# Kernel optimization log

Hardware: AMD Instinct MI355X
Metric: run time of the kernel (lower is better)

Reference implementation:

```python
import jax, jax.numpy as jnp
import numpy as np

N = 100000
E = 1600000

def _gcn_layer(x, row, col, W, b):
    # gather neighbor feats then scatter-add into destination rows
    agg = jax.ops.segment_sum(x[col], row, num_segments=N)  # [N, d]
    deg = jax.ops.segment_sum(jnp.ones((row.shape[0],), x.dtype), row, num_segments=N)
    deg = jnp.clip(deg, 1.0, None)[:, None]  # [N, 1]
    return (agg / deg + x) @ W + b

def setup_inputs() -> dict:
    key = jax.random.key(0)
    ks = jax.random.split(key, 6)
    x = jax.random.normal(ks[0], (N, 64), dtype=jnp.float32)
    edge_index = jax.random.randint(ks[1], (2, E), 0, N, dtype=jnp.int64)
    W1 = jax.random.normal(ks[2], (64, 128), dtype=jnp.float32) * 0.1
    b1 = jax.random.normal(ks[3], (128,), dtype=jnp.float32) * 0.1
    W2 = jax.random.normal(ks[4], (128, 64), dtype=jnp.float32) * 0.1
    b2 = jax.random.normal(ks[5], (64,), dtype=jnp.float32) * 0.1
    return {"x": x, "edge_index": edge_index, "W1": W1, "b1": b1, "W2": W2, "b2": b2}

def reference(x, edge_index, W1, b1, W2, b2):
    row, col = edge_index[0], edge_index[1]
    h = jax.nn.relu(_gcn_layer(x, row, col, W1, b1))
    h = _gcn_layer(h, row, col, W2, b2)
    return h
```

## Files before the change

kernel.cpp:

```cpp
#include <hip/hip_runtime.h>
#include <stdint.h>

#define WS_ALIGN(x) (((x) + 255) & ~(size_t)255)
#define CSR_CAP 64
#define RPB 512
#define CAPB 9216

typedef __attribute__((ext_vector_type(8))) unsigned short ushort8_t;
typedef __attribute__((ext_vector_type(8))) short short8_t;
typedef __attribute__((ext_vector_type(4))) float float4_t;

static __device__ __forceinline__ unsigned short f2bf(float f) {
    unsigned u = __float_as_uint(f);
    unsigned r = (u + 0x7FFFu + ((u >> 16) & 1u)) >> 16;
    return (unsigned short)r;
}
static __device__ __forceinline__ float bf2f(unsigned short s) {
    return __uint_as_float(((unsigned)s) << 16);
}

__global__ void detect_idx_kernel(const int* __restrict__ p, int* __restrict__ flagOr) {
    int t = threadIdx.x;
    int v = 0;
    for (int i = t; i < 2048; i += 256) v |= p[2 * i + 1];
    if (v) atomicOr(flagOr, v);
}

__global__ void init_cursor_kernel(int* __restrict__ gCursor, int nb) {
    int i = blockIdx.x * 256 + threadIdx.x;
    if (i < nb) gCursor[i] = i * CAPB;
}

__global__ __launch_bounds__(256) void bucket_kernel(
    const void* __restrict__ eidx, int E, const int* __restrict__ flagOr,
    int nb, int* __restrict__ gCursor, int2* __restrict__ staging) {
    __shared__ int cnt[256];
    __shared__ int base[256];
    int t = threadIdx.x;
    if (t < nb) cnt[t] = 0;
    __syncthreads();

    int e0 = (blockIdx.x * 256 + t) * 8;
    bool is64 = (*flagOr == 0);
    int m = E - e0; if (m > 8) m = 8; if (m < 0) m = 0;
    int r[8], bk[8], slot[8];
    for (int j = 0; j < m; ++j) {
        r[j] = is64 ? (int)((const long long*)eidx)[e0 + j]
                    : ((const int*)eidx)[e0 + j];
        bk[j] = r[j] >> 9;
        slot[j] = atomicAdd(&cnt[bk[j]], 1);
    }
    __syncthreads();
    if (t < nb) base[t] = atomicAdd(&gCursor[t], cnt[t]);
    __syncthreads();
    for (int j = 0; j < m; ++j) {
        int c = is64 ? (int)((const long long*)eidx)[E + e0 + j]
                     : ((const int*)eidx)[E + e0 + j];
        int dst = base[bk[j]] + slot[j];
        if (dst < (bk[j] + 1) * CAPB) staging[dst] = make_int2(r[j], c);
    }
}

__global__ __launch_bounds__(1024) void ell_kernel(
    const int2* __restrict__ staging, const int* __restrict__ gCursor,
    int* __restrict__ csr, int* __restrict__ deg, int N) {
    __shared__ int lcnt[RPB];
    int b = blockIdx.x, t = threadIdx.x;
    if (t < RPB) lcnt[t] = 0;
    __syncthreads();
    int start = b * CAPB;
    int end = gCursor[b];
    if (end > start + CAPB) end = start + CAPB;
    for (int i = start + t; i < end; i += 1024) {
        int2 rc = staging[i];
        int lr = rc.x - (b << 9);
        int slot = atomicAdd(&lcnt[lr], 1);
        if (slot < CSR_CAP) csr[(size_t)rc.x * CSR_CAP + slot] = rc.y;
    }
    __syncthreads();
    int r = (b << 9) + t;
    if (t < RPB && r < N) deg[r] = lcnt[t];
}

__global__ void xcast_kernel(const float4* __restrict__ x, ushort4* __restrict__ xb,
                             int n4) {
    int i = blockIdx.x * 256 + threadIdx.x;
    if (i >= n4) return;
    float4 f = x[i];
    ushort4 o;
    o.x = f2bf(f.x); o.y = f2bf(f.y); o.z = f2bf(f.z); o.w = f2bf(f.w);
    xb[i] = o;
}

__global__ __launch_bounds__(256) void agg_kernel(
    const unsigned short* __restrict__ xb, const int* __restrict__ deg,
    const int* __restrict__ csr, unsigned short* __restrict__ v, int N) {
    int tid = threadIdx.x;
    int w = tid >> 6, lane = tid & 63;
    int oct = lane >> 3, fo = lane & 7;
    int n = blockIdx.x * 4 + w;
    if (n >= N) return;
    int d = deg[n];
    if (d > CSR_CAP) d = CSR_CAP;
    const int* row = &csr[(size_t)n * CSR_CAP];

    float a0 = 0, a1 = 0, a2 = 0, a3 = 0, a4 = 0, a5 = 0, a6 = 0, a7 = 0;
    int nIter = (d + 7) >> 3;
    int it = 0;
    for (; it + 2 <= nIter; it += 2) {
        int k0 = it * 8 + oct, k1 = k0 + 8;
        int i0 = (k0 < d) ? row[k0] : N;
        int i1 = (k1 < d) ? row[k1] : N;
        ushort8_t f0 = *(const ushort8_t*)&xb[(size_t)i0 * 64 + fo * 8];
        ushort8_t f1 = *(const ushort8_t*)&xb[(size_t)i1 * 64 + fo * 8];
        a0 += bf2f(f0[0]) + bf2f(f1[0]); a1 += bf2f(f0[1]) + bf2f(f1[1]);
        a2 += bf2f(f0[2]) + bf2f(f1[2]); a3 += bf2f(f0[3]) + bf2f(f1[3]);
        a4 += bf2f(f0[4]) + bf2f(f1[4]); a5 += bf2f(f0[5]) + bf2f(f1[5]);
        a6 += bf2f(f0[6]) + bf2f(f1[6]); a7 += bf2f(f0[7]) + bf2f(f1[7]);
    }
    if (it < nIter) {
        int k0 = it * 8 + oct;
        int i0 = (k0 < d) ? row[k0] : N;
        ushort8_t f0 = *(const ushort8_t*)&xb[(size_t)i0 * 64 + fo * 8];
        a0 += bf2f(f0[0]); a1 += bf2f(f0[1]); a2 += bf2f(f0[2]); a3 += bf2f(f0[3]);
        a4 += bf2f(f0[4]); a5 += bf2f(f0[5]); a6 += bf2f(f0[6]); a7 += bf2f(f0[7]);
    }
    #define RED(m) a0 += __shfl_xor(a0, m); a1 += __shfl_xor(a1, m); \
                   a2 += __shfl_xor(a2, m); a3 += __shfl_xor(a3, m); \
                   a4 += __shfl_xor(a4, m); a5 += __shfl_xor(a5, m); \
                   a6 += __shfl_xor(a6, m); a7 += __shfl_xor(a7, m);
    RED(8) RED(16) RED(32)
    #undef RED

    if (oct == 0) {
        ushort8_t s = *(const ushort8_t*)&xb[(size_t)n * 64 + fo * 8];
        float inv = 1.0f / (float)(d > 1 ? d : 1);
        ushort8_t o;
        o[0] = f2bf(a0 * inv + bf2f(s[0])); o[1] = f2bf(a1 * inv + bf2f(s[1]));
        o[2] = f2bf(a2 * inv + bf2f(s[2])); o[3] = f2bf(a3 * inv + bf2f(s[3]));
        o[4] = f2bf(a4 * inv + bf2f(s[4])); o[5] = f2bf(a5 * inv + bf2f(s[5]));
        o[6] = f2bf(a6 * inv + bf2f(s[6])); o[7] = f2bf(a7 * inv + bf2f(s[7]));
        *(ushort8_t*)&v[(size_t)n * 64 + fo * 8] = o;
    }
}

__global__ __launch_bounds__(256) void mlp_kernel(
    const unsigned short* __restrict__ v, const float* __restrict__ W1,
    const float* __restrict__ b1, const float* __restrict__ W2,
    unsigned short* __restrict__ g16, int N) {
    __shared__ unsigned short vA[64 * 72];
    __shared__ unsigned short W1t[128 * 72];
    __shared__ unsigned short hA[64 * 136];
    __shared__ unsigned short W2t[64 * 136];
    int t = threadIdx.x;
    int node0 = blockIdx.x * 64;

    for (int i = t; i < 1024; i += 256) {
        int node = i >> 4, k0 = (i & 15) * 4;
        int gn = node0 + node;
        ushort4 val = make_ushort4(0, 0, 0, 0);
        if (gn < N) val = *(const ushort4*)&v[(size_t)gn * 64 + k0];
        *(ushort4*)&vA[node * 72 + k0] = val;
    }
    for (int i = t; i < 8192; i += 256) {
        int k = i >> 7, col = i & 127;
        W1t[col * 72 + k] = f2bf(W1[i]);
    }
    for (int i = t; i < 8192; i += 256) {
        int k = i >> 6, col = i & 63;
        W2t[col * 136 + k] = f2bf(W2[i]);
    }
    __syncthreads();

    int w = t >> 6, lane = t & 63;
    int l15 = lane & 15, quad = lane >> 4;
    const float4_t fzero = {0.f, 0.f, 0.f, 0.f};

    short8_t af[4][2];
    #pragma unroll
    for (int ms = 0; ms < 4; ++ms)
        #pragma unroll
        for (int kk = 0; kk < 2; ++kk)
            af[ms][kk] = *(const short8_t*)&vA[(ms * 16 + l15) * 72 + kk * 32 + quad * 8];
    short8_t bf1[2][2];
    #pragma unroll
    for (int cs = 0; cs < 2; ++cs)
        #pragma unroll
        for (int kk = 0; kk < 2; ++kk)
            bf1[cs][kk] = *(const short8_t*)&W1t[((w * 2 + cs) * 16 + l15) * 72 + kk * 32 + quad * 8];

    float4_t acc1[4][2];
    #pragma unroll
    for (int ms = 0; ms < 4; ++ms)
        #pragma unroll
        for (int cs = 0; cs < 2; ++cs)
            acc1[ms][cs] = fzero;
    #pragma unroll
    for (int ms = 0; ms < 4; ++ms)
        #pragma unroll
        for (int cs = 0; cs < 2; ++cs) {
            acc1[ms][cs] = __builtin_amdgcn_mfma_f32_16x16x32_bf16(af[ms][0], bf1[cs][0], acc1[ms][cs], 0, 0, 0);
            acc1[ms][cs] = __builtin_amdgcn_mfma_f32_16x16x32_bf16(af[ms][1], bf1[cs][1], acc1[ms][cs], 0, 0, 0);
        }

    #pragma unroll
    for (int cs = 0; cs < 2; ++cs) {
        int col = (w * 2 + cs) * 16 + l15;
        float bias = b1[col];
        #pragma unroll
        for (int ms = 0; ms < 4; ++ms) {
            #pragma unroll
            for (int r = 0; r < 4; ++r) {
                int node = ms * 16 + quad * 4 + r;
                hA[node * 136 + col] = f2bf(fmaxf(acc1[ms][cs][r] + bias, 0.f));
            }
        }
    }
    __syncthreads();

    short8_t bh[4];
    #pragma unroll
    for (int kk = 0; kk < 4; ++kk)
        bh[kk] = *(const short8_t*)&W2t[(w * 16 + l15) * 136 + kk * 32 + quad * 8];

    #pragma unroll
    for (int ms = 0; ms < 4; ++ms) {
        float4_t acc2 = fzero;
        #pragma unroll
        for (int kk = 0; kk < 4; ++kk) {
            short8_t ah = *(const short8_t*)&hA[(ms * 16 + l15) * 136 + kk * 32 + quad * 8];
            acc2 = __builtin_amdgcn_mfma_f32_16x16x32_bf16(ah, bh[kk], acc2, 0, 0, 0);
        }
        #pragma unroll
        for (int r = 0; r < 4; ++r) {
            int gn = node0 + ms * 16 + quad * 4 + r;
            if (gn < N) g16[(size_t)gn * 64 + w * 16 + l15] = f2bf(acc2[r]);
        }
    }
}

__global__ __launch_bounds__(256) void final_kernel(
    const unsigned short* __restrict__ g16, const float* __restrict__ b2,
    const int* __restrict__ deg, const int* __restrict__ csr,
    float* __restrict__ out, int N) {
    int tid = threadIdx.x;
    int w = tid >> 6, lane = tid & 63;
    int oct = lane >> 3, fo = lane & 7;
    int n = blockIdx.x * 4 + w;
    if (n >= N) return;
    int d = deg[n];
    if (d > CSR_CAP) d = CSR_CAP;
    const int* row = &csr[(size_t)n * CSR_CAP];

    float a0 = 0, a1 = 0, a2 = 0, a3 = 0, a4 = 0, a5 = 0, a6 = 0, a7 = 0;
    int nIter = (d + 7) >> 3;
    int it = 0;
    for (; it + 2 <= nIter; it += 2) {
        int k0 = it * 8 + oct, k1 = k0 + 8;
        int i0 = (k0 < d) ? row[k0] : N;
        int i1 = (k1 < d) ? row[k1] : N;
        ushort8_t f0 = *(const ushort8_t*)&g16[(size_t)i0 * 64 + fo * 8];
        ushort8_t f1 = *(const ushort8_t*)&g16[(size_t)i1 * 64 + fo * 8];
        a0 += bf2f(f0[0]) + bf2f(f1[0]); a1 += bf2f(f0[1]) + bf2f(f1[1]);
        a2 += bf2f(f0[2]) + bf2f(f1[2]); a3 += bf2f(f0[3]) + bf2f(f1[3]);
        a4 += bf2f(f0[4]) + bf2f(f1[4]); a5 += bf2f(f0[5]) + bf2f(f1[5]);
        a6 += bf2f(f0[6]) + bf2f(f1[6]); a7 += bf2f(f0[7]) + bf2f(f1[7]);
    }
    if (it < nIter) {
        int k0 = it * 8 + oct;
        int i0 = (k0 < d) ? row[k0] : N;
        ushort8_t f0 = *(const ushort8_t*)&g16[(size_t)i0 * 64 + fo * 8];
        a0 += bf2f(f0[0]); a1 += bf2f(f0[1]); a2 += bf2f(f0[2]); a3 += bf2f(f0[3]);
        a4 += bf2f(f0[4]); a5 += bf2f(f0[5]); a6 += bf2f(f0[6]); a7 += bf2f(f0[7]);
    }
    #define RED(m) a0 += __shfl_xor(a0, m); a1 += __shfl_xor(a1, m); \
                   a2 += __shfl_xor(a2, m); a3 += __shfl_xor(a3, m); \
                   a4 += __shfl_xor(a4, m); a5 += __shfl_xor(a5, m); \
                   a6 += __shfl_xor(a6, m); a7 += __shfl_xor(a7, m);
    RED(8) RED(16) RED(32)
    #undef RED

    if (oct == 0) {
        ushort8_t s = *(const ushort8_t*)&g16[(size_t)n * 64 + fo * 8];
        float4 bzA = ((const float4*)b2)[fo * 2];
        float4 bzB = ((const float4*)b2)[fo * 2 + 1];
        float inv = 1.0f / (float)(d > 1 ? d : 1);
        float4 oA, oB;
        oA.x = a0 * inv + bf2f(s[0]) + bzA.x;
        oA.y = a1 * inv + bf2f(s[1]) + bzA.y;
        oA.z = a2 * inv + bf2f(s[2]) + bzA.z;
        oA.w = a3 * inv + bf2f(s[3]) + bzA.w;
        oB.x = a4 * inv + bf2f(s[4]) + bzB.x;
        oB.y = a5 * inv + bf2f(s[5]) + bzB.y;
        oB.z = a6 * inv + bf2f(s[6]) + bzB.z;
        oB.w = a7 * inv + bf2f(s[7]) + bzB.w;
        *(float4*)&out[(size_t)n * 64 + fo * 8] = oA;
        *(float4*)&out[(size_t)n * 64 + fo * 8 + 4] = oB;
    }
}

extern "C" void kernel_launch(void* const* d_in, const int* in_sizes, int n_in,
                              void* d_out, int out_size, void* d_ws, size_t ws_size,
                              hipStream_t stream) {
    const float* x  = (const float*)d_in[0];
    const void*  ei = d_in[1];
    const float* W1 = (const float*)d_in[2];
    const float* b1 = (const float*)d_in[3];
    const float* W2 = (const float*)d_in[4];
    const float* b2 = (const float*)d_in[5];
    float* out = (float*)d_out;

    int N = out_size / 64;
    int E = in_sizes[1] / 2;
    int nb = (N + RPB - 1) / RPB;

    char* ws = (char*)d_ws;
    size_t off = 0;
    auto alloc = [&](size_t bytes) { size_t r = off; off += WS_ALIGN(bytes); return r; };
    int* flagOr  = (int*)(ws + alloc(4));
    int* gCursor = (int*)(ws + alloc((size_t)4 * nb));
    int* deg     = (int*)(ws + alloc((size_t)4 * N));
    int* csr     = (int*)(ws + alloc((size_t)4 * N * CSR_CAP));
    char* bufA   = ws + alloc((size_t)128 * (N + 1));
    unsigned short* xb  = (unsigned short*)bufA;
    unsigned short* g16 = (unsigned short*)bufA;
    unsigned short* v   = (unsigned short*)(ws + alloc((size_t)128 * N));
    int2* staging = (int2*)(ws + alloc((size_t)8 * nb * CAPB));
    (void)ws_size;

    hipMemsetAsync(flagOr, 0, 4, stream);
    hipMemsetAsync(bufA + (size_t)128 * N, 0, 128, stream);

    detect_idx_kernel<<<1, 256, 0, stream>>>((const int*)ei, flagOr);
    init_cursor_kernel<<<(nb + 255) / 256, 256, 0, stream>>>(gCursor, nb);

    int b1blocks = (E + 2047) / 2048;
    bucket_kernel<<<b1blocks, 256, 0, stream>>>(ei, E, flagOr, nb, gCursor, staging);
    ell_kernel<<<nb, 1024, 0, stream>>>(staging, gCursor, csr, deg, N);

    xcast_kernel<<<(N * 16 + 255) / 256, 256, 0, stream>>>((const float4*)x, (ushort4*)xb, N * 16);
    agg_kernel<<<(N + 3) / 4, 256, 0, stream>>>(xb, deg, csr, v, N);
    mlp_kernel<<<(N + 63) / 64, 256, 0, stream>>>(v, W1, b1, W2, g16, N);
    final_kernel<<<(N + 3) / 4, 256, 0, stream>>>(g16, b2, deg, csr, out, N);
}
```

Measured before the change: 251.4 us.

## Build ELL with global atomics, gather feature-per-lane, precast weights once

Replaces the two-pass bucket/staging ELL build with a single pass that takes a slot per edge from a global atomic counter on the degree array (zeroed by a memset). Rewrites both aggregation kernels so each lane owns one feature: neighbour indices are broadcast with readlane and the per-lane partial sums need no cross-lane shuffle reduction. Weight transposition and bf16 conversion move to a small separate kernel, so the MLP kernel reads MMA fragments straight from global memory and no longer fills LDS for every block. The risks are contention on the global atomics, 2-byte per-lane gathers in place of 16-byte vector loads, and uncached global fragment loads in the MLP.

```diff
diff --git a/kernel.cpp b/kernel.cpp
--- a/kernel.cpp
+++ b/kernel.cpp
@@ -3,8 +3,6 @@
 
 #define WS_ALIGN(x) (((x) + 255) & ~(size_t)255)
 #define CSR_CAP 64
-#define RPB 512
-#define CAPB 9216
 
 typedef __attribute__((ext_vector_type(8))) unsigned short ushort8_t;
 typedef __attribute__((ext_vector_type(8))) short short8_t;
@@ -26,60 +24,22 @@
     if (v) atomicOr(flagOr, v);
 }
 
-__global__ void init_cursor_kernel(int* __restrict__ gCursor, int nb) {
+__global__ __launch_bounds__(256) void fill_kernel(
+    const void* __restrict__ eidx, int E, const int* __restrict__ flagOr,
+    int* __restrict__ deg, int* __restrict__ csr) {
     int i = blockIdx.x * 256 + threadIdx.x;
-    if (i < nb) gCursor[i] = i * CAPB;
-}
-
-__global__ __launch_bounds__(256) void bucket_kernel(
-    const void* __restrict__ eidx, int E, const int* __restrict__ flagOr,
-    int nb, int* __restrict__ gCursor, int2* __restrict__ staging) {
-    __shared__ int cnt[256];
-    __shared__ int base[256];
-    int t = threadIdx.x;
-    if (t < nb) cnt[t] = 0;
-    __syncthreads();
-
-    int e0 = (blockIdx.x * 256 + t) * 8;
+    if (i >= E) return;
     bool is64 = (*flagOr == 0);
-    int m = E - e0; if (m > 8) m = 8; if (m < 0) m = 0;
-    int r[8], bk[8], slot[8];
-    for (int j = 0; j < m; ++j) {
-        r[j] = is64 ? (int)((const long long*)eidx)[e0 + j]
-                    : ((const int*)eidx)[e0 + j];
-        bk[j] = r[j] >> 9;
-        slot[j] = atomicAdd(&cnt[bk[j]], 1);
-    }
-    __syncthreads();
-    if (t < nb) base[t] = atomicAdd(&gCursor[t], cnt[t]);
-    __syncthreads();
-    for (int j = 0; j < m; ++j) {
-        int c = is64 ? (int)((const long long*)eidx)[E + e0 + j]
-                     : ((const int*)eidx)[E + e0 + j];
-        int dst = base[bk[j]] + slot[j];
-        if (dst < (bk[j] + 1) * CAPB) staging[dst] = make_int2(r[j], c);
-    }
-}
-
-__global__ __launch_bounds__(1024) void ell_kernel(
-    const int2* __restrict__ staging, const int* __restrict__ gCursor,
-    int* __restrict__ csr, int* __restrict__ deg, int N) {
-    __shared__ int lcnt[RPB];
-    int b = blockIdx.x, t = threadIdx.x;
-    if (t < RPB) lcnt[t] = 0;
-    __syncthreads();
-    int start = b * CAPB;
-    int end = gCursor[b];
-    if (end > start + CAPB) end = start + CAPB;
-    for (int i = start + t; i < end; i += 1024) {
-        int2 rc = staging[i];
-        int lr = rc.x - (b << 9);
-        int slot = atomicAdd(&lcnt[lr], 1);
-        if (slot < CSR_CAP) csr[(size_t)rc.x * CSR_CAP + slot] = rc.y;
-    }
-    __syncthreads();
-    int r = (b << 9) + t;
-    if (t < RPB && r < N) deg[r] = lcnt[t];
+    int r, c;
+    if (is64) {
+        r = (int)((const long long*)eidx)[i];
+        c = (int)((const long long*)eidx)[E + i];
+    } else {
+        r = ((const int*)eidx)[i];
+        c = ((const int*)eidx)[E + i];
+    }
+    int slot = atomicAdd(&deg[r], 1);
+    if (slot < CSR_CAP) csr[(size_t)r * CSR_CAP + slot] = c;
 }
 
 __global__ void xcast_kernel(const float4* __restrict__ x, ushort4* __restrict__ xb,
@@ -92,86 +52,71 @@
     xb[i] = o;
 }
 
+__global__ void wcast_kernel(const float* __restrict__ W1, const float* __restrict__ W2,
+                             unsigned short* __restrict__ W1t, unsigned short* __restrict__ W2t) {
+    int i = blockIdx.x * 256 + threadIdx.x;
+    if (i < 8192) {
+        int k = i >> 7, col = i & 127;
+        W1t[col * 64 + k] = f2bf(W1[i]);
+    } else if (i < 16384) {
+        int j = i - 8192;
+        int k = j >> 6, col = j & 63;
+        W2t[col * 128 + k] = f2bf(W2[j]);
+    }
+}
+
 __global__ __launch_bounds__(256) void agg_kernel(
     const unsigned short* __restrict__ xb, const int* __restrict__ deg,
     const int* __restrict__ csr, unsigned short* __restrict__ v, int N) {
     int tid = threadIdx.x;
     int w = tid >> 6, lane = tid & 63;
-    int oct = lane >> 3, fo = lane & 7;
     int n = blockIdx.x * 4 + w;
     if (n >= N) return;
     int d = deg[n];
     if (d > CSR_CAP) d = CSR_CAP;
-    const int* row = &csr[(size_t)n * CSR_CAP];
-
-    float a0 = 0, a1 = 0, a2 = 0, a3 = 0, a4 = 0, a5 = 0, a6 = 0, a7 = 0;
-    int nIter = (d + 7) >> 3;
+    int ri = csr[(size_t)n * CSR_CAP + lane];
+    if (lane >= d) ri = N;
+    int nIter = __builtin_amdgcn_readfirstlane((d + 7) >> 3);
+
+    float a0 = 0.f, a1 = 0.f, a2 = 0.f, a3 = 0.f;
+#define GL(J, KK) const unsigned short* bp##J = \
+        xb + ((size_t)(unsigned)__builtin_amdgcn_readlane(ri, (KK)) << 6); \
+        unsigned short t##J = bp##J[lane];
     int it = 0;
-    for (; it + 2 <= nIter; it += 2) {
-        int k0 = it * 8 + oct, k1 = k0 + 8;
-        int i0 = (k0 < d) ? row[k0] : N;
-        int i1 = (k1 < d) ? row[k1] : N;
-        ushort8_t f0 = *(const ushort8_t*)&xb[(size_t)i0 * 64 + fo * 8];
-        ushort8_t f1 = *(const ushort8_t*)&xb[(size_t)i1 * 64 + fo * 8];
-        a0 += bf2f(f0[0]) + bf2f(f1[0]); a1 += bf2f(f0[1]) + bf2f(f1[1]);
-        a2 += bf2f(f0[2]) + bf2f(f1[2]); a3 += bf2f(f0[3]) + bf2f(f1[3]);
-        a4 += bf2f(f0[4]) + bf2f(f1[4]); a5 += bf2f(f0[5]) + bf2f(f1[5]);
-        a6 += bf2f(f0[6]) + bf2f(f1[6]); a7 += bf2f(f0[7]) + bf2f(f1[7]);
-    }
-    if (it < nIter) {
-        int k0 = it * 8 + oct;
-        int i0 = (k0 < d) ? row[k0] : N;
-        ushort8_t f0 = *(const ushort8_t*)&xb[(size_t)i0 * 64 + fo * 8];
-        a0 += bf2f(f0[0]); a1 += bf2f(f0[1]); a2 += bf2f(f0[2]); a3 += bf2f(f0[3]);
-        a4 += bf2f(f0[4]); a5 += bf2f(f0[5]); a6 += bf2f(f0[6]); a7 += bf2f(f0[7]);
-    }
-    #define RED(m) a0 += __shfl_xor(a0, m); a1 += __shfl_xor(a1, m); \
-                   a2 += __shfl_xor(a2, m); a3 += __shfl_xor(a3, m); \
-                   a4 += __shfl_xor(a4, m); a5 += __shfl_xor(a5, m); \
-                   a6 += __shfl_xor(a6, m); a7 += __shfl_xor(a7, m);
-    RED(8) RED(16) RED(32)
-    #undef RED
-
-    if (oct == 0) {
-        ushort8_t s = *(const ushort8_t*)&xb[(size_t)n * 64 + fo * 8];
-        float inv = 1.0f / (float)(d > 1 ? d : 1);
-        ushort8_t o;
-        o[0] = f2bf(a0 * inv + bf2f(s[0])); o[1] = f2bf(a1 * inv + bf2f(s[1]));
-        o[2] = f2bf(a2 * inv + bf2f(s[2])); o[3] = f2bf(a3 * inv + bf2f(s[3]));
-        o[4] = f2bf(a4 * inv + bf2f(s[4])); o[5] = f2bf(a5 * inv + bf2f(s[5]));
-        o[6] = f2bf(a6 * inv + bf2f(s[6])); o[7] = f2bf(a7 * inv + bf2f(s[7]));
-        *(ushort8_t*)&v[(size_t)n * 64 + fo * 8] = o;
-    }
+    while (it < nIter) {
+        int k0 = it * 8;
+        if (nIter - it >= 2) {
+            GL(0, k0 + 0)  GL(1, k0 + 1)  GL(2, k0 + 2)  GL(3, k0 + 3)
+            GL(4, k0 + 4)  GL(5, k0 + 5)  GL(6, k0 + 6)  GL(7, k0 + 7)
+            GL(8, k0 + 8)  GL(9, k0 + 9)  GL(10, k0 + 10) GL(11, k0 + 11)
+            GL(12, k0 + 12) GL(13, k0 + 13) GL(14, k0 + 14) GL(15, k0 + 15)
+            a0 += bf2f(t0) + bf2f(t4);   a1 += bf2f(t1) + bf2f(t5);
+            a2 += bf2f(t2) + bf2f(t6);   a3 += bf2f(t3) + bf2f(t7);
+            a0 += bf2f(t8) + bf2f(t12);  a1 += bf2f(t9) + bf2f(t13);
+            a2 += bf2f(t10) + bf2f(t14); a3 += bf2f(t11) + bf2f(t15);
+            it += 2;
+        } else {
+            GL(16, k0 + 0) GL(17, k0 + 1) GL(18, k0 + 2) GL(19, k0 + 3)
+            GL(20, k0 + 4) GL(21, k0 + 5) GL(22, k0 + 6) GL(23, k0 + 7)
+            a0 += bf2f(t16); a1 += bf2f(t17); a2 += bf2f(t18); a3 += bf2f(t19);
+            a0 += bf2f(t20); a1 += bf2f(t21); a2 += bf2f(t22); a3 += bf2f(t23);
+            it += 1;
+        }
+    }
+#undef GL
+    float a = (a0 + a1) + (a2 + a3);
+    unsigned short s = xb[((size_t)n << 6) + lane];
+    float inv = 1.0f / (float)(d > 1 ? d : 1);
+    v[((size_t)n << 6) + lane] = f2bf(a * inv + bf2f(s));
 }
 
 __global__ __launch_bounds__(256) void mlp_kernel(
-    const unsigned short* __restrict__ v, const float* __restrict__ W1,
-    const float* __restrict__ b1, const float* __restrict__ W2,
+    const unsigned short* __restrict__ v, const unsigned short* __restrict__ W1t,
+    const float* __restrict__ b1, const unsigned short* __restrict__ W2t,
     unsigned short* __restrict__ g16, int N) {
-    __shared__ unsigned short vA[64 * 72];
-    __shared__ unsigned short W1t[128 * 72];
     __shared__ unsigned short hA[64 * 136];
-    __shared__ unsigned short W2t[64 * 136];
     int t = threadIdx.x;
     int node0 = blockIdx.x * 64;
-
-    for (int i = t; i < 1024; i += 256) {
-        int node = i >> 4, k0 = (i & 15) * 4;
-        int gn = node0 + node;
-        ushort4 val = make_ushort4(0, 0, 0, 0);
-        if (gn < N) val = *(const ushort4*)&v[(size_t)gn * 64 + k0];
-        *(ushort4*)&vA[node * 72 + k0] = val;
-    }
-    for (int i = t; i < 8192; i += 256) {
-        int k = i >> 7, col = i & 127;
-        W1t[col * 72 + k] = f2bf(W1[i]);
-    }
-    for (int i = t; i < 8192; i += 256) {
-        int k = i >> 6, col = i & 63;
-        W2t[col * 136 + k] = f2bf(W2[i]);
-    }
-    __syncthreads();
-
     int w = t >> 6, lane = t & 63;
     int l15 = lane & 15, quad = lane >> 4;
     const float4_t fzero = {0.f, 0.f, 0.f, 0.f};
@@ -181,13 +126,13 @@
     for (int ms = 0; ms < 4; ++ms)
         #pragma unroll
         for (int kk = 0; kk < 2; ++kk)
-            af[ms][kk] = *(const short8_t*)&vA[(ms * 16 + l15) * 72 + kk * 32 + quad * 8];
+            af[ms][kk] = *(const short8_t*)&v[(size_t)(node0 + ms * 16 + l15) * 64 + kk * 32 + quad * 8];
     short8_t bf1[2][2];
     #pragma unroll
     for (int cs = 0; cs < 2; ++cs)
         #pragma unroll
         for (int kk = 0; kk < 2; ++kk)
-            bf1[cs][kk] = *(const short8_t*)&W1t[((w * 2 + cs) * 16 + l15) * 72 + kk * 32 + quad * 8];
+            bf1[cs][kk] = *(const short8_t*)&W1t[((w * 2 + cs) * 16 + l15) * 64 + kk * 32 + quad * 8];
 
     float4_t acc1[4][2];
     #pragma unroll
@@ -221,7 +166,7 @@
     short8_t bh[4];
     #pragma unroll
     for (int kk = 0; kk < 4; ++kk)
-        bh[kk] = *(const short8_t*)&W2t[(w * 16 + l15) * 136 + kk * 32 + quad * 8];
+        bh[kk] = *(const short8_t*)&W2t[(w * 16 + l15) * 128 + kk * 32 + quad * 8];
 
     #pragma unroll
     for (int ms = 0; ms < 4; ++ms) {
@@ -245,58 +190,44 @@
     float* __restrict__ out, int N) {
     int tid = threadIdx.x;
     int w = tid >> 6, lane = tid & 63;
-    int oct = lane >> 3, fo = lane & 7;
     int n = blockIdx.x * 4 + w;
     if (n >= N) return;
     int d = deg[n];
     if (d > CSR_CAP) d = CSR_CAP;
-    const int* row = &csr[(size_t)n * CSR_CAP];
-
-    float a0 = 0, a1 = 0, a2 = 0, a3 = 0, a4 = 0, a5 = 0, a6 = 0, a7 = 0;
-    int nIter = (d + 7) >> 3;
+    int ri = csr[(size_t)n * CSR_CAP + lane];
+    if (lane >= d) ri = N;
+    int nIter = __builtin_amdgcn_readfirstlane((d + 7) >> 3);
+
+    float a0 = 0.f, a1 = 0.f, a2 = 0.f, a3 = 0.f;
+#define GL(J, KK) const unsigned short* bp##J = \
+        g16 + ((size_t)(unsigned)__builtin_amdgcn_readlane(ri, (KK)) << 6); \
+        unsigned short t##J = bp##J[lane];
     int it = 0;
-    for (; it + 2 <= nIter; it += 2) {
-        int k0 = it * 8 + oct, k1 = k0 + 8;
-        int i0 = (k0 < d) ? row[k0] : N;
-        int i1 = (k1 < d) ? row[k1] : N;
-        ushort8_t f0 = *(const ushort8_t*)&g16[(size_t)i0 * 64 + fo * 8];
-        ushort8_t f1 = *(const ushort8_t*)&g16[(size_t)i1 * 64 + fo * 8];
-        a0 += bf2f(f0[0]) + bf2f(f1[0]); a1 += bf2f(f0[1]) + bf2f(f1[1]);
-        a2 += bf2f(f0[2]) + bf2f(f1[2]); a3 += bf2f(f0[3]) + bf2f(f1[3]);
-        a4 += bf2f(f0[4]) + bf2f(f1[4]); a5 += bf2f(f0[5]) + bf2f(f1[5]);
-        a6 += bf2f(f0[6]) + bf2f(f1[6]); a7 += bf2f(f0[7]) + bf2f(f1[7]);
-    }
-    if (it < nIter) {
-        int k0 = it * 8 + oct;
-        int i0 = (k0 < d) ? row[k0] : N;
-        ushort8_t f0 = *(const ushort8_t*)&g16[(size_t)i0 * 64 + fo * 8];
-        a0 += bf2f(f0[0]); a1 += bf2f(f0[1]); a2 += bf2f(f0[2]); a3 += bf2f(f0[3]);
-        a4 += bf2f(f0[4]); a5 += bf2f(f0[5]); a6 += bf2f(f0[6]); a7 += bf2f(f0[7]);
-    }
-    #define RED(m) a0 += __shfl_xor(a0, m); a1 += __shfl_xor(a1, m); \
-                   a2 += __shfl_xor(a2, m); a3 += __shfl_xor(a3, m); \
-                   a4 += __shfl_xor(a4, m); a5 += __shfl_xor(a5, m); \
-                   a6 += __shfl_xor(a6, m); a7 += __shfl_xor(a7, m);
-    RED(8) RED(16) RED(32)
-    #undef RED
-
-    if (oct == 0) {
-        ushort8_t s = *(const ushort8_t*)&g16[(size_t)n * 64 + fo * 8];
-        float4 bzA = ((const float4*)b2)[fo * 2];
-        float4 bzB = ((const float4*)b2)[fo * 2 + 1];
-        float inv = 1.0f / (float)(d > 1 ? d : 1);
-        float4 oA, oB;
-        oA.x = a0 * inv + bf2f(s[0]) + bzA.x;
-        oA.y = a1 * inv + bf2f(s[1]) + bzA.y;
-        oA.z = a2 * inv + bf2f(s[2]) + bzA.z;
-        oA.w = a3 * inv + bf2f(s[3]) + bzA.w;
-        oB.x = a4 * inv + bf2f(s[4]) + bzB.x;
-        oB.y = a5 * inv + bf2f(s[5]) + bzB.y;
-        oB.z = a6 * inv + bf2f(s[6]) + bzB.z;
-        oB.w = a7 * inv + bf2f(s[7]) + bzB.w;
-        *(float4*)&out[(size_t)n * 64 + fo * 8] = oA;
-        *(float4*)&out[(size_t)n * 64 + fo * 8 + 4] = oB;
-    }
+    while (it < nIter) {
+        int k0 = it * 8;
+        if (nIter - it >= 2) {
+            GL(0, k0 + 0)  GL(1, k0 + 1)  GL(2, k0 + 2)  GL(3, k0 + 3)
+            GL(4, k0 + 4)  GL(5, k0 + 5)  GL(6, k0 + 6)  GL(7, k0 + 7)
+            GL(8, k0 + 8)  GL(9, k0 + 9)  GL(10, k0 + 10) GL(11, k0 + 11)
+            GL(12, k0 + 12) GL(13, k0 + 13) GL(14, k0 + 14) GL(15, k0 + 15)
+            a0 += bf2f(t0) + bf2f(t4);   a1 += bf2f(t1) + bf2f(t5);
+            a2 += bf2f(t2) + bf2f(t6);   a3 += bf2f(t3) + bf2f(t7);
+            a0 += bf2f(t8) + bf2f(t12);  a1 += bf2f(t9) + bf2f(t13);
+            a2 += bf2f(t10) + bf2f(t14); a3 += bf2f(t11) + bf2f(t15);
+            it += 2;
+        } else {
+            GL(16, k0 + 0) GL(17, k0 + 1) GL(18, k0 + 2) GL(19, k0 + 3)
+            GL(20, k0 + 4) GL(21, k0 + 5) GL(22, k0 + 6) GL(23, k0 + 7)
+            a0 += bf2f(t16); a1 += bf2f(t17); a2 += bf2f(t18); a3 += bf2f(t19);
+            a0 += bf2f(t20); a1 += bf2f(t21); a2 += bf2f(t22); a3 += bf2f(t23);
+            it += 1;
+        }
+    }
+#undef GL
+    float a = (a0 + a1) + (a2 + a3);
+    unsigned short s = g16[((size_t)n << 6) + lane];
+    float inv = 1.0f / (float)(d > 1 ? d : 1);
+    out[((size_t)n << 6) + lane] = a * inv + bf2f(s) + b2[lane];
 }
 
 extern "C" void kernel_launch(void* const* d_in, const int* in_sizes, int n_in,
@@ -312,34 +243,31 @@
 
     int N = out_size / 64;
     int E = in_sizes[1] / 2;
-    int nb = (N + RPB - 1) / RPB;
 
     char* ws = (char*)d_ws;
     size_t off = 0;
     auto alloc = [&](size_t bytes) { size_t r = off; off += WS_ALIGN(bytes); return r; };
     int* flagOr  = (int*)(ws + alloc(4));
-    int* gCursor = (int*)(ws + alloc((size_t)4 * nb));
     int* deg     = (int*)(ws + alloc((size_t)4 * N));
     int* csr     = (int*)(ws + alloc((size_t)4 * N * CSR_CAP));
     char* bufA   = ws + alloc((size_t)128 * (N + 1));
     unsigned short* xb  = (unsigned short*)bufA;
     unsigned short* g16 = (unsigned short*)bufA;
-    unsigned short* v   = (unsigned short*)(ws + alloc((size_t)128 * N));
-    int2* staging = (int2*)(ws + alloc((size_t)8 * nb * CAPB));
+    unsigned short* v   = (unsigned short*)(ws + alloc((size_t)128 * (N + 64)));
+    unsigned short* W1t = (unsigned short*)(ws + alloc((size_t)2 * 8192));
+    unsigned short* W2t = (unsigned short*)(ws + alloc((size_t)2 * 8192));
     (void)ws_size;
 
     hipMemsetAsync(flagOr, 0, 4, stream);
+    hipMemsetAsync(deg, 0, (size_t)4 * N, stream);
     hipMemsetAsync(bufA + (size_t)128 * N, 0, 128, stream);
 
     detect_idx_kernel<<<1, 256, 0, stream>>>((const int*)ei, flagOr);
-    init_cursor_kernel<<<(nb + 255) / 256, 256, 0, stream>>>(gCursor, nb);
-
-    int b1blocks = (E + 2047) / 2048;
-    bucket_kernel<<<b1blocks, 256, 0, stream>>>(ei, E, flagOr, nb, gCursor, staging);
-    ell_kernel<<<nb, 1024, 0, stream>>>(staging, gCursor, csr, deg, N);
+    fill_kernel<<<(E + 255) / 256, 256, 0, stream>>>(ei, E, flagOr, deg, csr);
 
     xcast_kernel<<<(N * 16 + 255) / 256, 256, 0, stream>>>((const float4*)x, (ushort4*)xb, N * 16);
+    wcast_kernel<<<64, 256, 0, stream>>>(W1, W2, W1t, W2t);
     agg_kernel<<<(N + 3) / 4, 256, 0, stream>>>(xb, deg, csr, v, N);
-    mlp_kernel<<<(N + 63) / 64, 256, 0, stream>>>(v, W1, b1, W2, g16, N);
+    mlp_kernel<<<(N + 63) / 64, 256, 0, stream>>>(v, W1t, b1, W2t, g16, N);
     final_kernel<<<(N + 3) / 4, 256, 0, stream>>>(g16, b2, deg, csr, out, N);
 }
```

Result: slower. 329.7 us (+31.2%).
